# Optimization experiments

Measured on AMD Instinct MI355X. Metric: run time of the kernel, lower is better.

## Reference

```python
import jax, jax.numpy as jnp
import numpy as np

N, U, K, S = 1024, 64, 2, 2        # nodes, rnn_units, max_diffusion_step, num_supports
Q = S * K + 1                       # diffusion matrices (incl. identity)
B, T, H = 64, 12, 12                # batch, seq_len, horizon
IN, OUT, L = 1, 1, 2                # input_dim, output_dim, num_rnn_layers


def setup_inputs() -> dict:
    key = jax.random.key(0)
    ks = jax.random.split(key, 16)

    def glorot(k, shape):
        fan = shape[0] + shape[-1]
        return jax.random.normal(k, shape, jnp.float32) * np.float32(np.sqrt(2.0 / fan))

    # random-walk supports from a random dense adjacency (DCRNN: transpose of D^-1 A)
    adj = jax.random.uniform(ks[0], (N, N), jnp.float32)
    rw = lambda a: a / a.sum(axis=1, keepdims=True)
    supports = jnp.stack([rw(adj).T, rw(adj.T).T])  # (S, N, N)

    inputs = jax.random.normal(ks[1], (B, N * IN, T), jnp.float32)

    p = {}
    i = 2
    for pre, ind in (("enc", IN), ("dec", OUT)):
        for l in range(L):
            f = (ind if l == 0 else U) + U
            p[f"{pre}_gw{l}"] = glorot(ks[i], (Q * f, 2 * U)); i += 1
            p[f"{pre}_gb{l}"] = jnp.ones((2 * U,), jnp.float32)   # GRU gate bias init 1.0
            p[f"{pre}_cw{l}"] = glorot(ks[i], (Q * f, U)); i += 1
            p[f"{pre}_cb{l}"] = jnp.zeros((U,), jnp.float32)
    p["proj_w"] = glorot(ks[i], (U, OUT))
    p["proj_b"] = jnp.zeros((OUT,), jnp.float32)
    return {"inputs": inputs, "supports": supports, **p}


def _diffusion(x, supports):
    # x: (B, N, F) -> (B, N, Q*F); Chebyshev-style recurrence as in DCGRUCell._gconv
    mats = [x]
    for s in range(S):
        A = supports[s]
        x0 = x
        x1 = jnp.einsum('nm,bmf->bnf', A, x0)
        mats.append(x1)
        for _ in range(2, K + 1):
            x2 = 2.0 * jnp.einsum('nm,bmf->bnf', A, x1) - x0
            mats.append(x2)
            x0, x1 = x1, x2
    return jnp.concatenate(mats, axis=-1)


def _cell(x, h, supports, gw, gb, cw, cb):
    # x: (B,N,Fin), h: (B,N,U)
    ru = jax.nn.sigmoid(_diffusion(jnp.concatenate([x, h], -1), supports) @ gw + gb)
    r, u = ru[..., :U], ru[..., U:]
    c = jnp.tanh(_diffusion(jnp.concatenate([x, r * h], -1), supports) @ cw + cb)
    return u * h + (1.0 - u) * c


def reference(inputs, supports,
              enc_gw0, enc_gb0, enc_cw0, enc_cb0,
              enc_gw1, enc_gb1, enc_cw1, enc_cb1,
              dec_gw0, dec_gb0, dec_cw0, dec_cb0,
              dec_gw1, dec_gb1, dec_cw1, dec_cb1,
              proj_w, proj_b):
    enc = [(enc_gw0, enc_gb0, enc_cw0, enc_cb0), (enc_gw1, enc_gb1, enc_cw1, enc_cb1)]
    dec = [(dec_gw0, dec_gb0, dec_cw0, dec_cb0), (dec_gw1, dec_gb1, dec_cw1, dec_cb1)]

    x_seq = inputs.reshape(B, N, IN, T).transpose(3, 0, 1, 2)  # (T, B, N, IN)
    h0 = jnp.zeros((L, B, N, U), inputs.dtype)

    def enc_step(h, x):
        out, hs = x, []
        for l in range(L):
            hn = _cell(out, h[l], supports, *enc[l])
            hs.append(hn)
            out = hn
        return jnp.stack(hs), None

    hT, _ = jax.lax.scan(enc_step, h0, x_seq)

    def dec_step(carry, _):
        h, xin = carry
        out, hs = xin, []
        for l in range(L):
            hn = _cell(out, h[l], supports, *dec[l])
            hs.append(hn)
            out = hn
        proj = out @ proj_w + proj_b          # (B, N, OUT)
        return (jnp.stack(hs), proj), proj.reshape(B, N * OUT)

    go = jnp.zeros((B, N, OUT), inputs.dtype)
    _, outs = jax.lax.scan(dec_step, (hT, go), None, length=H)
    return outs  # (H, B, N*OUT)
```

## Files before the change

### kernel.cpp

```cpp
#include <hip/hip_runtime.h>

typedef _Float16 f16;
typedef _Float16 f16x4 __attribute__((ext_vector_type(4)));
typedef _Float16 f16x8 __attribute__((ext_vector_type(8)));
typedef float    f32x4 __attribute__((ext_vector_type(4)));

#define NN 1024
#define NT 12
#define NHOR 12
#define ROWS (NN*64)
static const long SLOT = (long)NN*4096;

__device__ __forceinline__ int swz(int row, int halfoff) {
  return row*32 + ((((halfoff>>3) ^ row) & 3)<<3) + (halfoff&7);
}

template<int NR>
__device__ __forceinline__ void stage_rows(f16* lds, const f16* src, long ldk, int k0, int w, int l) {
  const int r4 = l>>2, c4 = l&3;
  #pragma unroll
  for (int ic=0; ic<NR/64; ++ic) {
    const int row = (w + ic*4)*16 + r4;
    const f16* g = src + (long)row*ldk + k0 + ((c4 ^ (row&3))<<3);
    f16* d = lds + row*32 + c4*8;
    __builtin_amdgcn_global_load_lds((const __attribute__((address_space(1))) void*)g,
                                     (__attribute__((address_space(3))) void*)d, 16, 0, 0);
  }
}

__device__ __forceinline__ f16x8 frag(const f16* lds, int row, int lk) {
  f16x4 lo = *(const f16x4*)&lds[swz(row, lk)];
  f16x4 hi = *(const f16x4*)&lds[swz(row, 16+lk)];
  f16x8 r; r[0]=lo[0];r[1]=lo[1];r[2]=lo[2];r[3]=lo[3];
  r[4]=hi[0];r[5]=hi[1];r[6]=hi[2];r[7]=hi[3];
  return r;
}

struct DiffP {
  const f16* A0; const f16* A1; int nt0;
  const f16* B;
  f16* out0; f16* out1;
  long ldo1;
  int mode_x;
  int wsq;
};

__global__ __launch_bounds__(256) void gemm_diff(DiffP p) {
  __shared__ f16 As[128*32];
  __shared__ f16 Bs[128*32];
  const int tid=threadIdx.x, l=tid&63, w=tid>>6;
  const int rq=l>>4, ro=l&15, lk=rq*4;
  const int rt=blockIdx.x, ct=blockIdx.y;
  const int part = (rt >= p.nt0);
  const int rtl  = part ? (rt - p.nt0) : rt;
  const f16* Abase = (part ? p.A1 : p.A0) + (long)rtl*128*1024;
  const f16* Bbase = p.B + (long)ct*128*1024;
  const int wm=(w>>1)*64, wc=(w&1)*64;
  f32x4 acc[4][4] = {};
  for (int k0=0; k0<1024; k0+=32) {
    stage_rows<128>(As, Abase, 1024, k0, w, l);
    stage_rows<128>(Bs, Bbase, 1024, k0, w, l);
    __syncthreads();
    f16x8 a[4], b[4];
    #pragma unroll
    for (int i=0;i<4;i++) a[i] = frag(As, wm + i*16 + ro, lk);
    #pragma unroll
    for (int j=0;j<4;j++) b[j] = frag(Bs, wc + j*16 + ro, lk);
    #pragma unroll
    for (int i=0;i<4;i++)
      #pragma unroll
      for (int j=0;j<4;j++)
        acc[i][j] = __builtin_amdgcn_mfma_f32_16x16x32_f16(a[i], b[j], acc[i][j], 0,0,0);
    __syncthreads();
  }
  const int c0 = ct*128;
  if (p.wsq) {
    #pragma unroll
    for (int i=0;i<4;i++)
      #pragma unroll
      for (int j=0;j<4;j++) {
        const int cg = c0 + wc + j*16 + ro;
        #pragma unroll
        for (int e=0;e<4;e++) {
          const long rg = (long)rt*128 + wm + i*16 + rq*4 + e;
          float v = 2.f*acc[i][j][e] - ((rg==cg)?1.f:0.f);
          p.out0[rg*p.ldo1 + cg] = (f16)v;
        }
      }
    return;
  }
  f16* ob = part ? p.out1 : p.out0;
  const int mode = part ? p.mode_x : 0;
  #pragma unroll
  for (int i=0;i<4;i++) {
    const int crow = rtl*128 + wm + i*16 + rq*4;
    #pragma unroll
    for (int j=0;j<4;j++) {
      const int col = c0 + wc + j*16 + ro;
      const int q = col>>10, n = col&1023;
      f16x4 sv;
      #pragma unroll
      for (int e=0;e<4;e++) sv[e] = (f16)acc[i][j][e];
      if (mode == 0)          *(f16x4*)(ob + (long)q*SLOT + (long)n*4096 + crow) = sv;
      else if (crow < 64)     *(f16x4*)(ob + (long)q*ROWS + n*64 + crow) = sv;
    }
  }
}

struct Tab5 { const f16* p[5]; };
struct CellP {
  Tab5 ta, tb, xq;
  const f16 *wa, *wb, *wx0;
  const float* bias;
  const float* h32in;
  f16* rh; float* u32;
  float* h32io; f16* h16io;
  int nseg, xf1;
};

template<int O, int GATE>
__global__ __launch_bounds__(256) void cell_gemm(CellP p) {
  constexpr int FC = O/32;
  __shared__ f16 As[128*32];
  __shared__ f16 Bs[O*32];
  const int tid=threadIdx.x, l=tid&63, w=tid>>6;
  const int rq=l>>4, ro=l&15, lk=rq*4;
  const int wm=(w>>1)*64, wc=(w&1)*(O/2);
  f32x4 acc[4][FC] = {};
  const long r0 = (long)blockIdx.x*128;
  const int Ktot = p.nseg*320;
  for (int kg=0; kg<Ktot; kg+=32) {
    const int seg = (kg>=320) ? 1 : 0;
    const int kk  = kg - seg*320;
    const int q = kk>>6, kq = kk&63;
    const f16* asrc = (seg ? p.tb.p[q] : p.ta.p[q]) + r0*64;
    const f16* wsrc = seg ? p.wb : p.wa;
    stage_rows<128>(As, asrc, 64, kq, w, l);
    stage_rows<O>(Bs, wsrc, 320, kk, w, l);
    __syncthreads();
    f16x8 a[4], b[FC];
    #pragma unroll
    for (int i=0;i<4;i++) a[i] = frag(As, wm + i*16 + ro, lk);
    #pragma unroll
    for (int j=0;j<FC;j++) b[j] = frag(Bs, wc + j*16 + ro, lk);
    #pragma unroll
    for (int i=0;i<4;i++)
      #pragma unroll
      for (int j=0;j<FC;j++)
        acc[i][j] = __builtin_amdgcn_mfma_f32_16x16x32_f16(a[i], b[j], acc[i][j], 0,0,0);
    __syncthreads();
  }
  #pragma unroll
  for (int i=0;i<4;i++) {
    #pragma unroll
    for (int e=0;e<4;e++) {
      const long rg = r0 + wm + i*16 + rq*4 + e;
      float xv[5];
      if (p.xf1) {
        #pragma unroll
        for (int q2=0;q2<5;q2++) xv[q2] = (float)p.xq.p[q2][rg];
      }
      #pragma unroll
      for (int j=0;j<FC;j++) {
        const int col = wc + j*16 + ro;
        float v = acc[i][j][e] + p.bias[col];
        if (p.xf1) {
          #pragma unroll
          for (int q2=0;q2<5;q2++) v += xv[q2] * (float)p.wx0[q2*O + col];
        }
        if (GATE) {
          const float s = 1.f/(1.f + __expf(-v));
          if (col < 64) p.rh[rg*64 + col] = (f16)(s * p.h32in[rg*64 + col]);
          else          p.u32[rg*64 + (col-64)] = s;
        } else {
          const float cc = tanhf(v);
          const float u  = p.u32[rg*64 + col];
          const float h  = p.h32io[rg*64 + col];
          const float hn = u*h + (1.f-u)*cc;
          p.h32io[rg*64 + col] = hn;
          p.h16io[rg*64 + col] = (f16)hn;
        }
      }
    }
  }
}

__global__ __launch_bounds__(256) void k_transpose(const f16* in, f16* out, int R, int C) {
  __shared__ f16 T[64*66];
  const long rb = (long)blockIdx.x*64, cb = (long)blockIdx.y*64;
  const int t = threadIdx.x;
  #pragma unroll
  for (int it=0; it<2; ++it) {
    const int r = (t>>3) + it*32, c8 = (t&7)*8;
    f16x8 v = *(const f16x8*)(in + (rb+r)*C + cb + c8);
    *(f16x8*)&T[r*66 + c8] = v;
  }
  __syncthreads();
  #pragma unroll
  for (int it=0; it<2; ++it) {
    const int c = (t>>3) + it*32, r8 = (t&7)*8;
    f16x8 v;
    #pragma unroll
    for (int j=0;j<8;j++) v[j] = T[(r8+j)*66 + c];
    *(f16x8*)(out + (cb+c)*R + rb + r8) = v;
  }
}

__global__ void k_cast_sup(const float* s, f16* W) {
  long i = (long)blockIdx.x*256 + threadIdx.x;
  if (i >= 2LL*NN*NN) return;
  long ss = (i >= (long)NN*NN) ? 1 : 0;
  long off = i - ss*(long)NN*NN;
  W[ss*2*(long)NN*NN + off] = (f16)s[i];
}

__global__ void k_pack_x(const float* in, f16* xe, f16* xet) {
  int i = blockIdx.x*256 + threadIdx.x;
  if (i >= NT*ROWS) return;
  int t = i / ROWS, r = i % ROWS, n = r>>6, b = r&63;
  float v = in[(long)b*NN*NT + (long)n*NT + t];
  xe[i] = (f16)v;
  xet[(long)t*128*1024 + (long)b*1024 + n] = (f16)v;
}

__global__ void k_split_w_t(const float* src, f16* wh_t, f16* wxA, int f, int xf, int O) {
  int i = blockIdx.x*256 + threadIdx.x;
  if (i >= 5*f*O) return;
  int o = i % O, rr = i / O, q = rr / f, ff = rr % f;
  f16 v = (f16)src[i];
  if (ff < xf) {
    if (xf == 1) wxA[q*O + o] = v;
    else         wxA[(long)o*320 + q*64 + ff] = v;
  } else {
    wh_t[(long)o*320 + q*64 + (ff - xf)] = v;
  }
}

__global__ void k_proj(const float* h32, const float* pw, const float* pb,
                       float* out, f16* xdec, f16* xdect) {
  int r = blockIdx.x*256 + threadIdx.x;
  if (r >= ROWS) return;
  float acc = pb[0];
  const float* hp = h32 + (long)r*64;
  #pragma unroll
  for (int k=0;k<64;k++) acc += hp[k]*pw[k];
  int n = r>>6, b = r&63;
  out[(long)b*NN + n] = acc;
  xdec[r] = (f16)acc;
  xdect[(long)b*1024 + n] = (f16)acc;
}

extern "C" void kernel_launch(void* const* d_in, const int* in_sizes, int n_in,
                              void* d_out, int out_size, void* d_ws, size_t ws_size,
                              hipStream_t stream) {
  (void)in_sizes; (void)n_in; (void)out_size; (void)ws_size;
  const float* inputs = (const float*)d_in[0];
  const float* sup    = (const float*)d_in[1];
  const float* gwp[4] = {(const float*)d_in[2], (const float*)d_in[6], (const float*)d_in[10], (const float*)d_in[14]};
  const float* gbp[4] = {(const float*)d_in[3], (const float*)d_in[7], (const float*)d_in[11], (const float*)d_in[15]};
  const float* cwp[4] = {(const float*)d_in[4], (const float*)d_in[8], (const float*)d_in[12], (const float*)d_in[16]};
  const float* cbp[4] = {(const float*)d_in[5], (const float*)d_in[9], (const float*)d_in[13], (const float*)d_in[17]};
  const float* pw = (const float*)d_in[18];
  const float* pb = (const float*)d_in[19];
  float* out = (float*)d_out;

  char* base = (char*)d_ws; size_t off = 0;
  auto alloc = [&](size_t bytes)->void* { void* p = base + off; off += (bytes + 255) & ~(size_t)255; return p; };
  f16* W16    = (f16*)alloc(4LL*NN*NN*2);
  f16* xenc   = (f16*)alloc((long)NT*ROWS*2);
  f16* xenct  = (f16*)alloc((long)NT*128*1024*2);
  f16* xdec   = (f16*)alloc((long)ROWS*2);
  f16* xdect  = (f16*)alloc(128L*1024*2);
  f16*  h16[2]  = {(f16*)alloc((long)ROWS*64*2),  (f16*)alloc((long)ROWS*64*2)};
  f16*  hhat[2] = {(f16*)alloc(4096L*1024*2),     (f16*)alloc(4096L*1024*2)};
  float* h32[2] = {(float*)alloc((long)ROWS*64*4), (float*)alloc((long)ROWS*64*4)};
  float* u32 = (float*)alloc((long)ROWS*64*4);
  f16* rh    = (f16*)alloc((long)ROWS*64*2);
  f16* rhhat = (f16*)alloc(4096L*1024*2);
  f16* Dh    = (f16*)alloc(4*SLOT*2);
  f16* Dx    = (f16*)alloc(4*SLOT*2);
  f16* Dx0   = (f16*)alloc(4LL*ROWS*2);
  f16 *gwh[4], *gwx[4], *cwh[4], *cwx[4];
  for (int i=0;i<4;i++) {
    gwh[i]=(f16*)alloc(128L*320*2); gwx[i]=(f16*)alloc(128L*320*2);
    cwh[i]=(f16*)alloc(64L*320*2);  cwx[i]=(f16*)alloc(64L*320*2);
  }

  hipMemsetAsync(h16[0], 0, (long)ROWS*64*2, stream);
  hipMemsetAsync(h16[1], 0, (long)ROWS*64*2, stream);
  hipMemsetAsync(hhat[0], 0, 4096L*1024*2, stream);
  hipMemsetAsync(hhat[1], 0, 4096L*1024*2, stream);
  hipMemsetAsync(h32[0], 0, (long)ROWS*64*4, stream);
  hipMemsetAsync(h32[1], 0, (long)ROWS*64*4, stream);
  hipMemsetAsync(xdec,   0, (long)ROWS*2, stream);
  hipMemsetAsync(xdect,  0, 128L*1024*2, stream);

  k_cast_sup<<<(2*NN*NN+255)/256, 256, 0, stream>>>(sup, W16);
  f16* At = Dh;
  for (int s=0;s<2;s++)
    k_transpose<<<dim3(16,16),256,0,stream>>>(W16 + (long)s*2*NN*NN, At + (long)s*NN*NN, 1024, 1024);
  for (int s=0;s<2;s++) {
    DiffP mp{};
    mp.A0 = W16 + (long)s*2*NN*NN; mp.A1 = mp.A0; mp.nt0 = 8;
    mp.B  = At + (long)s*NN*NN;
    mp.out0 = W16 + ((long)s*2+1)*NN*NN; mp.ldo1 = 1024; mp.wsq = 1;
    gemm_diff<<<dim3(8,8),256,0,stream>>>(mp);
  }
  k_pack_x<<<(NT*ROWS+255)/256,256,0,stream>>>(inputs, xenc, xenct);
  const int fs[4]  = {65,128,65,128};
  const int xfs[4] = {1,64,1,64};
  for (int i=0;i<4;i++) {
    k_split_w_t<<<(5*fs[i]*128+255)/256,256,0,stream>>>(gwp[i], gwh[i], gwx[i], fs[i], xfs[i], 128);
    k_split_w_t<<<(5*fs[i]*64 +255)/256,256,0,stream>>>(cwp[i], cwh[i], cwx[i], fs[i], xfs[i], 64);
  }

  auto run_cell = [&](const f16* xraw, const f16* xhat, int xf,
                      f16* h16c, f16* hhatc, float* h32c, int wi) {
    DiffP dp{};
    dp.A0 = hhatc; dp.nt0 = 32; dp.B = W16; dp.out0 = Dh;
    int gx;
    if (xf == 64) { dp.A1 = xhat; dp.out1 = Dx;  dp.mode_x = 0; gx = 64; }
    else          { dp.A1 = xhat; dp.out1 = Dx0; dp.mode_x = 2; gx = 33; }
    gemm_diff<<<dim3(gx, 32), 256, 0, stream>>>(dp);
    CellP gp{};
    gp.ta.p[0] = h16c; for (int q=1;q<5;q++) gp.ta.p[q] = Dh + (long)(q-1)*SLOT;
    gp.wa = gwh[wi]; gp.bias = gbp[wi];
    gp.h32in = h32c; gp.rh = rh; gp.u32 = u32;
    if (xf == 64) {
      gp.nseg = 2; gp.xf1 = 0;
      gp.tb.p[0] = xraw; for (int q=1;q<5;q++) gp.tb.p[q] = Dx + (long)(q-1)*SLOT;
      gp.wb = gwx[wi];
    } else {
      gp.nseg = 1; gp.xf1 = 1;
      gp.xq.p[0] = xraw; for (int q=1;q<5;q++) gp.xq.p[q] = Dx0 + (long)(q-1)*ROWS;
      gp.wx0 = gwx[wi];
    }
    cell_gemm<128,1><<<512, 256, 0, stream>>>(gp);
    k_transpose<<<dim3(16,64),256,0,stream>>>(rh, rhhat, 1024, 4096);
    DiffP dp2{};
    dp2.A0 = rhhat; dp2.A1 = rhhat; dp2.nt0 = 32; dp2.B = W16; dp2.out0 = Dh;
    gemm_diff<<<dim3(32, 32), 256, 0, stream>>>(dp2);
    CellP cp{};
    cp.ta.p[0] = rh; for (int q=1;q<5;q++) cp.ta.p[q] = Dh + (long)(q-1)*SLOT;
    cp.wa = cwh[wi]; cp.bias = cbp[wi];
    cp.u32 = u32; cp.h32io = h32c; cp.h16io = h16c;
    if (xf == 64) {
      cp.nseg = 2; cp.xf1 = 0;
      cp.tb.p[0] = xraw; for (int q=1;q<5;q++) cp.tb.p[q] = Dx + (long)(q-1)*SLOT;
      cp.wb = cwx[wi];
    } else {
      cp.nseg = 1; cp.xf1 = 1;
      cp.xq.p[0] = xraw; for (int q=1;q<5;q++) cp.xq.p[q] = Dx0 + (long)(q-1)*ROWS;
      cp.wx0 = cwx[wi];
    }
    cell_gemm<64,0><<<512, 256, 0, stream>>>(cp);
    k_transpose<<<dim3(16,64),256,0,stream>>>(h16c, hhatc, 1024, 4096);
  };

  for (int t=0;t<NT;t++) {
    run_cell(xenc + (long)t*ROWS, xenct + (long)t*128*1024, 1, h16[0], hhat[0], h32[0], 0);
    run_cell(h16[0], hhat[0],                              64, h16[1], hhat[1], h32[1], 1);
  }
  for (int s=0;s<NHOR;s++) {
    run_cell(xdec,   xdect,   1, h16[0], hhat[0], h32[0], 2);
    run_cell(h16[0], hhat[0],64, h16[1], hhat[1], h32[1], 3);
    k_proj<<<ROWS/256, 256, 0, stream>>>(h32[1], pw, pb, out + (long)s*ROWS, xdec, xdect);
  }
}
```

Before: 10.93 ms.

## Read hidden state via LDS transpose loads and interleave K layout to drop transposes

The diffusion GEMM now reads the node-major hidden state directly and transposes it in LDS with ds_read_b64_tr_b16, so the per-cell k_transpose kernels and the hhat/rhhat buffers are no longer needed. Supports, weights and x-hat are pre-permuted with an interleaved K ordering, which lets fragments load as a single 16-byte LDS read instead of two 8-byte reads. MFMA operand order is swapped and epilogue stores are rewritten to match. This removes two transpose launches and their memory traffic per cell, but adds scattered scalar f16 stores in the epilogue and depends on the correctness of the new swizzles.

```diff
diff --git a/kernel.cpp b/kernel.cpp
--- a/kernel.cpp
+++ b/kernel.cpp
@@ -9,38 +9,49 @@
 #define NT 12
 #define NHOR 12
 #define ROWS (NN*64)
+#define MATH (1024*1024)
 static const long SLOT = (long)NN*4096;
 
-__device__ __forceinline__ int swz(int row, int halfoff) {
-  return row*32 + ((((halfoff>>3) ^ row) & 3)<<3) + (halfoff&7);
+__device__ __forceinline__ int sw4(int row){ return (row ^ (row>>2)) & 3; }
+
+__device__ __forceinline__ int ilvpos(int k){
+  int r = k & 31;
+  return (k & ~31) + ((r & 12) << 1) + (r & 3) + ((r & 16) >> 2);
 }
 
 template<int NR>
-__device__ __forceinline__ void stage_rows(f16* lds, const f16* src, long ldk, int k0, int w, int l) {
-  const int r4 = l>>2, c4 = l&3;
-  #pragma unroll
-  for (int ic=0; ic<NR/64; ++ic) {
-    const int row = (w + ic*4)*16 + r4;
-    const f16* g = src + (long)row*ldk + k0 + ((c4 ^ (row&3))<<3);
-    f16* d = lds + row*32 + c4*8;
+__device__ __forceinline__ void stage(f16* lds, const f16* src, int ldk, int k0, int tid){
+  #pragma unroll
+  for (int ic=0; ic<NR/64; ++ic){
+    const int c = tid + ic*256;
+    const int row = c>>2, c4 = c&3;
+    const f16* g = src + (long)row*ldk + k0 + ((c4 ^ sw4(row))<<3);
+    f16* d = lds + c*8;
     __builtin_amdgcn_global_load_lds((const __attribute__((address_space(1))) void*)g,
                                      (__attribute__((address_space(3))) void*)d, 16, 0, 0);
   }
 }
 
-__device__ __forceinline__ f16x8 frag(const f16* lds, int row, int lk) {
-  f16x4 lo = *(const f16x4*)&lds[swz(row, lk)];
-  f16x4 hi = *(const f16x4*)&lds[swz(row, 16+lk)];
+__device__ __forceinline__ f16x8 fragI(const f16* lds, int row, int rq){
+  return *(const f16x8*)&lds[row*32 + ((rq ^ sw4(row))<<3)];
+}
+
+__device__ __forceinline__ f16x8 fragN(const f16* lds, int row, int lk){
+  const int s = sw4(row);
+  const int cl = (lk>>3) ^ s, ch = (2|(lk>>3)) ^ s;
+  f16x4 lo = *(const f16x4*)&lds[row*32 + (cl<<3) + (lk&7)];
+  f16x4 hi = *(const f16x4*)&lds[row*32 + (ch<<3) + (lk&7)];
   f16x8 r; r[0]=lo[0];r[1]=lo[1];r[2]=lo[2];r[3]=lo[3];
   r[4]=hi[0];r[5]=hi[1];r[6]=hi[2];r[7]=hi[3];
   return r;
 }
 
 struct DiffP {
-  const f16* A0; const f16* A1; int nt0;
+  const f16* A0; const f16* A1;
   const f16* B;
   f16* out0; f16* out1;
-  long ldo1;
+  int nt0;
+  int a0tr, a1tr;
   int mode_x;
   int wsq;
 };
@@ -53,56 +64,90 @@
   const int rt=blockIdx.x, ct=blockIdx.y;
   const int part = (rt >= p.nt0);
   const int rtl  = part ? (rt - p.nt0) : rt;
-  const f16* Abase = (part ? p.A1 : p.A0) + (long)rtl*128*1024;
+  const int atr  = part ? p.a1tr : p.a0tr;
+  const f16* Ab  = part ? p.A1 : p.A0;
   const f16* Bbase = p.B + (long)ct*128*1024;
   const int wm=(w>>1)*64, wc=(w&1)*64;
+  const int n_t  = ((tid>>5)&1)*16 + ((tid>>3)&3)*4 + ((tid>>1)&3);
+  const int but0 = ((tid>>6)&3)*16 + (tid&1)*8;
+  const f16* gtr = Ab + (long)n_t*4096 + (long)rtl*128 + but0;
+  const f16* Ailv = Ab + (long)rtl*128*1024;
   f32x4 acc[4][4] = {};
   for (int k0=0; k0<1024; k0+=32) {
-    stage_rows<128>(As, Abase, 1024, k0, w, l);
-    stage_rows<128>(Bs, Bbase, 1024, k0, w, l);
+    if (atr) {
+      const f16* g = gtr + (long)k0*4096;
+      __builtin_amdgcn_global_load_lds((const __attribute__((address_space(1))) void*)g,
+                                       (__attribute__((address_space(3))) void*)(As + tid*8), 16, 0, 0);
+      __builtin_amdgcn_global_load_lds((const __attribute__((address_space(1))) void*)(g + 64),
+                                       (__attribute__((address_space(3))) void*)(As + (tid+256)*8), 16, 0, 0);
+    } else {
+      stage<128>(As, Ailv, 1024, k0, tid);
+    }
+    stage<128>(Bs, Bbase, 1024, k0, tid);
     __syncthreads();
     f16x8 a[4], b[4];
-    #pragma unroll
-    for (int i=0;i<4;i++) a[i] = frag(As, wm + i*16 + ro, lk);
-    #pragma unroll
-    for (int j=0;j<4;j++) b[j] = frag(Bs, wc + j*16 + ro, lk);
+    if (atr) {
+      const unsigned abase = (unsigned)(size_t)(__attribute__((address_space(3))) f16*)&As[0]
+                           + (unsigned)((w>>1)*4096 + l*8);
+      f16x4 tlo[4], thi[4];
+      #pragma unroll
+      for (int i=0;i<4;i++){
+        asm volatile("ds_read_b64_tr_b16 %0, %1 offset:%2" : "=v"(tlo[i]) : "v"(abase), "i"(i*1024));
+        asm volatile("ds_read_b64_tr_b16 %0, %1 offset:%2" : "=v"(thi[i]) : "v"(abase), "i"(i*1024+512));
+      }
+      asm volatile("s_waitcnt lgkmcnt(0)" ::: "memory");
+      __builtin_amdgcn_sched_barrier(0);
+      #pragma unroll
+      for (int i=0;i<4;i++){
+        f16x8 t2; t2[0]=tlo[i][0];t2[1]=tlo[i][1];t2[2]=tlo[i][2];t2[3]=tlo[i][3];
+        t2[4]=thi[i][0];t2[5]=thi[i][1];t2[6]=thi[i][2];t2[7]=thi[i][3];
+        a[i]=t2;
+      }
+    } else {
+      #pragma unroll
+      for (int i=0;i<4;i++) a[i] = fragI(As, wm + i*16 + ro, rq);
+    }
+    #pragma unroll
+    for (int j=0;j<4;j++) b[j] = fragI(Bs, wc + j*16 + ro, rq);
     #pragma unroll
     for (int i=0;i<4;i++)
       #pragma unroll
       for (int j=0;j<4;j++)
-        acc[i][j] = __builtin_amdgcn_mfma_f32_16x16x32_f16(a[i], b[j], acc[i][j], 0,0,0);
+        acc[i][j] = __builtin_amdgcn_mfma_f32_16x16x32_f16(b[j], a[i], acc[i][j], 0,0,0);
     __syncthreads();
   }
-  const int c0 = ct*128;
   if (p.wsq) {
     #pragma unroll
-    for (int i=0;i<4;i++)
-      #pragma unroll
-      for (int j=0;j<4;j++) {
-        const int cg = c0 + wc + j*16 + ro;
+    for (int i=0;i<4;i++){
+      const long rg = (long)rt*128 + wm + i*16 + ro;
+      #pragma unroll
+      for (int j=0;j<4;j++){
+        const int cb = ct*128 + wc + j*16 + lk;
+        f16x4 sv;
         #pragma unroll
-        for (int e=0;e<4;e++) {
-          const long rg = (long)rt*128 + wm + i*16 + rq*4 + e;
-          float v = 2.f*acc[i][j][e] - ((rg==cg)?1.f:0.f);
-          p.out0[rg*p.ldo1 + cg] = (f16)v;
-        }
-      }
+        for (int e=0;e<4;e++) sv[e] = (f16)(2.f*acc[i][j][e] - ((rg==(long)(cb+e))?1.f:0.f));
+        *(f16x4*)&p.out0[rg*1024 + cb] = sv;
+      }
+    }
     return;
   }
   f16* ob = part ? p.out1 : p.out0;
   const int mode = part ? p.mode_x : 0;
-  #pragma unroll
-  for (int i=0;i<4;i++) {
-    const int crow = rtl*128 + wm + i*16 + rq*4;
-    #pragma unroll
-    for (int j=0;j<4;j++) {
-      const int col = c0 + wc + j*16 + ro;
-      const int q = col>>10, n = col&1023;
-      f16x4 sv;
-      #pragma unroll
-      for (int e=0;e<4;e++) sv[e] = (f16)acc[i][j][e];
-      if (mode == 0)          *(f16x4*)(ob + (long)q*SLOT + (long)n*4096 + crow) = sv;
-      else if (crow < 64)     *(f16x4*)(ob + (long)q*ROWS + n*64 + crow) = sv;
+  const long rowbase = (long)rtl*128;
+  #pragma unroll
+  for (int i=0;i<4;i++){
+    const int bu = wm + i*16 + ro;
+    if (mode==2 && bu>=64) continue;
+    #pragma unroll
+    for (int j=0;j<4;j++){
+      const int cb = ct*128 + wc + j*16 + lk;
+      #pragma unroll
+      for (int e=0;e<4;e++){
+        const int c = cb + e, q = c>>10, n = c&1023;
+        const f16 v = (f16)acc[i][j][e];
+        if (mode==0) ob[(long)q*SLOT + (long)n*4096 + rowbase + bu] = v;
+        else         ob[(long)q*ROWS + n*64 + bu] = v;
+      }
     }
   }
 }
@@ -135,14 +180,14 @@
     const int q = kk>>6, kq = kk&63;
     const f16* asrc = (seg ? p.tb.p[q] : p.ta.p[q]) + r0*64;
     const f16* wsrc = seg ? p.wb : p.wa;
-    stage_rows<128>(As, asrc, 64, kq, w, l);
-    stage_rows<O>(Bs, wsrc, 320, kk, w, l);
+    stage<128>(As, asrc, 64, kq, tid);
+    stage<O>(Bs, wsrc, 320, kk, tid);
     __syncthreads();
     f16x8 a[4], b[FC];
     #pragma unroll
-    for (int i=0;i<4;i++) a[i] = frag(As, wm + i*16 + ro, lk);
-    #pragma unroll
-    for (int j=0;j<FC;j++) b[j] = frag(Bs, wc + j*16 + ro, lk);
+    for (int i=0;i<4;i++) a[i] = fragN(As, wm + i*16 + ro, lk);
+    #pragma unroll
+    for (int j=0;j<FC;j++) b[j] = fragI(Bs, wc + j*16 + ro, rq);
     #pragma unroll
     for (int i=0;i<4;i++)
       #pragma unroll
@@ -206,12 +251,16 @@
   }
 }
 
-__global__ void k_cast_sup(const float* s, f16* W) {
+__global__ void k_cast_sup(const float* s, f16* o) {
   long i = (long)blockIdx.x*256 + threadIdx.x;
-  if (i >= 2LL*NN*NN) return;
-  long ss = (i >= (long)NN*NN) ? 1 : 0;
-  long off = i - ss*(long)NN*NN;
-  W[ss*2*(long)NN*NN + off] = (f16)s[i];
+  if (i < 2LL*MATH) o[i] = (f16)s[i];
+}
+
+__global__ void k_ilv(const f16* in, f16* out) {
+  int i = blockIdx.x*256 + threadIdx.x;
+  if (i >= MATH) return;
+  int r = i>>10, k = i&1023;
+  out[(long)r*1024 + ilvpos(k)] = in[i];
 }
 
 __global__ void k_pack_x(const float* in, f16* xe, f16* xet) {
@@ -220,7 +269,7 @@
   int t = i / ROWS, r = i % ROWS, n = r>>6, b = r&63;
   float v = in[(long)b*NN*NT + (long)n*NT + t];
   xe[i] = (f16)v;
-  xet[(long)t*128*1024 + (long)b*1024 + n] = (f16)v;
+  xet[(long)t*131072 + (long)b*1024 + ilvpos(n)] = (f16)v;
 }
 
 __global__ void k_split_w_t(const float* src, f16* wh_t, f16* wxA, int f, int xf, int O) {
@@ -230,9 +279,9 @@
   f16 v = (f16)src[i];
   if (ff < xf) {
     if (xf == 1) wxA[q*O + o] = v;
-    else         wxA[(long)o*320 + q*64 + ff] = v;
+    else         wxA[(long)o*320 + q*64 + ilvpos(ff)] = v;
   } else {
-    wh_t[(long)o*320 + q*64 + (ff - xf)] = v;
+    wh_t[(long)o*320 + q*64 + ilvpos(ff - xf)] = v;
   }
 }
 
@@ -247,7 +296,7 @@
   int n = r>>6, b = r&63;
   out[(long)b*NN + n] = acc;
   xdec[r] = (f16)acc;
-  xdect[(long)b*1024 + n] = (f16)acc;
+  xdect[(long)b*1024 + ilvpos(n)] = (f16)acc;
 }
 
 extern "C" void kernel_launch(void* const* d_in, const int* in_sizes, int n_in,
@@ -266,17 +315,15 @@
 
   char* base = (char*)d_ws; size_t off = 0;
   auto alloc = [&](size_t bytes)->void* { void* p = base + off; off += (bytes + 255) & ~(size_t)255; return p; };
-  f16* W16    = (f16*)alloc(4LL*NN*NN*2);
+  f16* W16int = (f16*)alloc(4LL*MATH*2);
   f16* xenc   = (f16*)alloc((long)NT*ROWS*2);
-  f16* xenct  = (f16*)alloc((long)NT*128*1024*2);
+  f16* xet    = (f16*)alloc((long)NT*131072*2);
   f16* xdec   = (f16*)alloc((long)ROWS*2);
-  f16* xdect  = (f16*)alloc(128L*1024*2);
+  f16* xdect  = (f16*)alloc(131072L*2);
   f16*  h16[2]  = {(f16*)alloc((long)ROWS*64*2),  (f16*)alloc((long)ROWS*64*2)};
-  f16*  hhat[2] = {(f16*)alloc(4096L*1024*2),     (f16*)alloc(4096L*1024*2)};
   float* h32[2] = {(float*)alloc((long)ROWS*64*4), (float*)alloc((long)ROWS*64*4)};
   float* u32 = (float*)alloc((long)ROWS*64*4);
   f16* rh    = (f16*)alloc((long)ROWS*64*2);
-  f16* rhhat = (f16*)alloc(4096L*1024*2);
   f16* Dh    = (f16*)alloc(4*SLOT*2);
   f16* Dx    = (f16*)alloc(4*SLOT*2);
   f16* Dx0   = (f16*)alloc(4LL*ROWS*2);
@@ -288,25 +335,29 @@
 
   hipMemsetAsync(h16[0], 0, (long)ROWS*64*2, stream);
   hipMemsetAsync(h16[1], 0, (long)ROWS*64*2, stream);
-  hipMemsetAsync(hhat[0], 0, 4096L*1024*2, stream);
-  hipMemsetAsync(hhat[1], 0, 4096L*1024*2, stream);
   hipMemsetAsync(h32[0], 0, (long)ROWS*64*4, stream);
   hipMemsetAsync(h32[1], 0, (long)ROWS*64*4, stream);
   hipMemsetAsync(xdec,   0, (long)ROWS*2, stream);
-  hipMemsetAsync(xdect,  0, 128L*1024*2, stream);
-
-  k_cast_sup<<<(2*NN*NN+255)/256, 256, 0, stream>>>(sup, W16);
-  f16* At = Dh;
-  for (int s=0;s<2;s++)
-    k_transpose<<<dim3(16,16),256,0,stream>>>(W16 + (long)s*2*NN*NN, At + (long)s*NN*NN, 1024, 1024);
+  hipMemsetAsync(xdect,  0, 131072L*2, stream);
+
+  f16* tmpA   = Dh;
+  f16* tmpAt  = Dh + 2L*MATH;
+  f16* tmpAti = Dh + 4L*MATH;
+  f16* tmpSq  = Dh + 5L*MATH;
+  k_cast_sup<<<(2*MATH+255)/256, 256, 0, stream>>>(sup, tmpA);
   for (int s=0;s<2;s++) {
+    k_transpose<<<dim3(16,16),256,0,stream>>>(tmpA + (long)s*MATH, tmpAt + (long)s*MATH, 1024, 1024);
+    k_ilv<<<4096,256,0,stream>>>(tmpA + (long)s*MATH, W16int + (long)(2*s)*MATH);
+  }
+  for (int s=0;s<2;s++) {
+    k_ilv<<<4096,256,0,stream>>>(tmpAt + (long)s*MATH, tmpAti);
     DiffP mp{};
-    mp.A0 = W16 + (long)s*2*NN*NN; mp.A1 = mp.A0; mp.nt0 = 8;
-    mp.B  = At + (long)s*NN*NN;
-    mp.out0 = W16 + ((long)s*2+1)*NN*NN; mp.ldo1 = 1024; mp.wsq = 1;
+    mp.A0 = W16int + (long)(2*s)*MATH; mp.A1 = mp.A0; mp.a0tr = 0; mp.a1tr = 0; mp.nt0 = 8;
+    mp.B = tmpAti; mp.out0 = tmpSq; mp.wsq = 1;
     gemm_diff<<<dim3(8,8),256,0,stream>>>(mp);
-  }
-  k_pack_x<<<(NT*ROWS+255)/256,256,0,stream>>>(inputs, xenc, xenct);
+    k_ilv<<<4096,256,0,stream>>>(tmpSq, W16int + (long)(2*s+1)*MATH);
+  }
+  k_pack_x<<<(NT*ROWS+255)/256,256,0,stream>>>(inputs, xenc, xet);
   const int fs[4]  = {65,128,65,128};
   const int xfs[4] = {1,64,1,64};
   for (int i=0;i<4;i++) {
@@ -314,13 +365,13 @@
     k_split_w_t<<<(5*fs[i]*64 +255)/256,256,0,stream>>>(cwp[i], cwh[i], cwx[i], fs[i], xfs[i], 64);
   }
 
-  auto run_cell = [&](const f16* xraw, const f16* xhat, int xf,
-                      f16* h16c, f16* hhatc, float* h32c, int wi) {
+  auto run_cell = [&](const f16* xraw, const f16* xA, int xf,
+                      f16* h16c, float* h32c, int wi) {
     DiffP dp{};
-    dp.A0 = hhatc; dp.nt0 = 32; dp.B = W16; dp.out0 = Dh;
+    dp.A0 = h16c; dp.a0tr = 1; dp.nt0 = 32; dp.B = W16int; dp.out0 = Dh; dp.wsq = 0;
     int gx;
-    if (xf == 64) { dp.A1 = xhat; dp.out1 = Dx;  dp.mode_x = 0; gx = 64; }
-    else          { dp.A1 = xhat; dp.out1 = Dx0; dp.mode_x = 2; gx = 33; }
+    if (xf == 64) { dp.A1 = xA; dp.a1tr = 1; dp.out1 = Dx;  dp.mode_x = 0; gx = 64; }
+    else          { dp.A1 = xA; dp.a1tr = 0; dp.out1 = Dx0; dp.mode_x = 2; gx = 33; }
     gemm_diff<<<dim3(gx, 32), 256, 0, stream>>>(dp);
     CellP gp{};
     gp.ta.p[0] = h16c; for (int q=1;q<5;q++) gp.ta.p[q] = Dh + (long)(q-1)*SLOT;
@@ -336,9 +387,9 @@
       gp.wx0 = gwx[wi];
     }
     cell_gemm<128,1><<<512, 256, 0, stream>>>(gp);
-    k_transpose<<<dim3(16,64),256,0,stream>>>(rh, rhhat, 1024, 4096);
     DiffP dp2{};
-    dp2.A0 = rhhat; dp2.A1 = rhhat; dp2.nt0 = 32; dp2.B = W16; dp2.out0 = Dh;
+    dp2.A0 = rh; dp2.a0tr = 1; dp2.A1 = rh; dp2.a1tr = 1; dp2.nt0 = 32;
+    dp2.B = W16int; dp2.out0 = Dh; dp2.wsq = 0;
     gemm_diff<<<dim3(32, 32), 256, 0, stream>>>(dp2);
     CellP cp{};
     cp.ta.p[0] = rh; for (int q=1;q<5;q++) cp.ta.p[q] = Dh + (long)(q-1)*SLOT;
@@ -354,16 +405,15 @@
       cp.wx0 = cwx[wi];
     }
     cell_gemm<64,0><<<512, 256, 0, stream>>>(cp);
-    k_transpose<<<dim3(16,64),256,0,stream>>>(h16c, hhatc, 1024, 4096);
   };
 
   for (int t=0;t<NT;t++) {
-    run_cell(xenc + (long)t*ROWS, xenct + (long)t*128*1024, 1, h16[0], hhat[0], h32[0], 0);
-    run_cell(h16[0], hhat[0],                              64, h16[1], hhat[1], h32[1], 1);
+    run_cell(xenc + (long)t*ROWS, xet + (long)t*131072, 1, h16[0], h32[0], 0);
+    run_cell(h16[0], h16[0],                           64, h16[1], h32[1], 1);
   }
   for (int s=0;s<NHOR;s++) {
-    run_cell(xdec,   xdect,   1, h16[0], hhat[0], h32[0], 2);
-    run_cell(h16[0], hhat[0],64, h16[1], hhat[1], h32[1], 3);
+    run_cell(xdec,   xdect,   1, h16[0], h32[0], 2);
+    run_cell(h16[0], h16[0], 64, h16[1], h32[1], 3);
     k_proj<<<ROWS/256, 256, 0, stream>>>(h32[1], pw, pb, out + (long)s*ROWS, xdec, xdect);
   }
 }
```

New measurement: 11.00 ms. About the same (+0.7%).
